# Kernel optimization log

Measured on AMD Instinct MI355X. Metric: run time of the kernel, lower is better.

## Reference

```python
import jax, jax.numpy as jnp
import numpy as np

L = 32      # num_layer
N_ORD = 64  # order_of_a_LTImodel
U = 64      # u_size
Y = 64      # y_size
T = 8192    # sequence length
SCALE = 0.05  # keep block-bidiagonal A spectrally stable over 8192 steps


def setup_inputs() -> dict:
    key = jax.random.key(0)
    k_u, k_a, k_b0, k_bl, k_c = jax.random.split(key, 5)
    inp = {
        "input": jax.random.normal(k_u, (T, U), dtype=jnp.float32),
        # per-layer A_i weights (diagonal blocks)
        "A_stack": jax.random.normal(k_a, (L, N_ORD, N_ORD), dtype=jnp.float32) * SCALE,
        # layer-0 B (maps u -> state)
        "B0": jax.random.normal(k_b0, (N_ORD, U), dtype=jnp.float32) * SCALE,
        # layer i>=1 B weights (sub-diagonal coupling blocks)
        "B_lower": jax.random.normal(k_bl, (L - 1, N_ORD, N_ORD), dtype=jnp.float32) * SCALE,
        # per-layer C_i weights, concatenated along columns in forward
        "C_stack": jax.random.normal(k_c, (L, Y, N_ORD), dtype=jnp.float32),
        # D is frozen zeros (feedthrough=False)
        "D_w": jnp.zeros((Y, U), dtype=jnp.float32),
    }
    return inp


def _assemble(A_stack, B0, B_lower, C_stack):
    l, n, _ = A_stack.shape
    S = l * n
    A = jnp.zeros((S, S), A_stack.dtype)
    for i in range(l):  # fixed small structural loop
        A = A.at[i * n:(i + 1) * n, i * n:(i + 1) * n].set(A_stack[i])
    for i in range(1, l):
        A = A.at[i * n:(i + 1) * n, (i - 1) * n:i * n].set(B_lower[i - 1])
    B = jnp.concatenate([B0, jnp.zeros((S - n, B0.shape[1]), B0.dtype)], axis=0)
    # torch.cat([C_i], dim=1): [Y, L*n]
    C = jnp.transpose(C_stack, (1, 0, 2)).reshape(C_stack.shape[1], S)
    return A, B, C


def reference(input, A_stack, B0, B_lower, C_stack, D_w):
    A, B, C = _assemble(A_stack, B0, B_lower, C_stack)
    S = A.shape[0]
    x0 = jnp.zeros((S,), input.dtype)

    def step(x, u):
        y = C @ x + D_w @ u      # output BEFORE state update (y_t uses x_t)
        x_next = A @ x + B @ u
        return x_next, y

    _, ys = jax.lax.scan(step, x0, input)
    return ys  # [T, Y]
```

## Files before the change

kernel.cpp:

```cpp
#include <hip/hip_runtime.h>


#define NO   64
#define TSEQ 8192
#define PAD8 40
#define PRX  8240
#define PBX  ((size_t)PRX*NO)
#define KQ   2048

typedef _Float16 h16;
typedef _Float16 h16x8 __attribute__((ext_vector_type(8)));
typedef float    f32x4 __attribute__((ext_vector_type(4)));

#define MFMA16(a,b,c) __builtin_amdgcn_mfma_f32_16x16x32_f16((a),(b),(c),0,0,0)
#define IMAX(a,b) ((a)>(b)?(a):(b))
#define IMIN(a,b) ((a)<(b)?(a):(b))

__global__ __launch_bounds__(256) void prep_build(
    const float* __restrict__ u, const float* __restrict__ B0,
    const float* __restrict__ Bl, const float* __restrict__ Cst,
    const float* __restrict__ Ast,
    h16* __restrict__ xq, h16* __restrict__ ccast,
    h16* __restrict__ SN, h16* __restrict__ ST,
    float* __restrict__ Dacc)
{
    __shared__ __align__(16) h16   Ah[64*72];
    __shared__ __align__(16) h16   kT[64*72];
    __shared__ __align__(16) float kf[64*68];
    const int tid = threadIdx.x;

    if (blockIdx.x < 32) {
        const int layer = blockIdx.x;
        const bool wantST = (layer & 3) == 0;
        const float* k0 = (layer == 0) ? B0 : (Bl + (size_t)(layer-1)*4096);
        const float* Aw = Ast + (size_t)layer*4096;
        for (int e8 = tid; e8 < 512; e8 += 256) {
            int n = e8 >> 3, m0 = (e8 & 7) << 3;
            f32x4 a0 = *(const f32x4*)&Aw[n*64 + m0];
            f32x4 a1 = *(const f32x4*)&Aw[n*64 + m0 + 4];
            h16 ah[8];
            #pragma unroll
            for (int t = 0; t < 4; t++) { ah[t] = (h16)a0[t]; ah[4+t] = (h16)a1[t]; }
            *(int4*)&Ah[n*72 + m0] = *(int4*)&ah[0];
            *(f32x4*)&kf[n*68 + m0]     = *(const f32x4*)&k0[n*64 + m0];
            *(f32x4*)&kf[n*68 + m0 + 4] = *(const f32x4*)&k0[n*64 + m0 + 4];
        }
        __syncthreads();
        const int wv = tid >> 6, lane = tid & 63, r = lane & 15, q = lane >> 4;
        const h16x8 a0 = *(const h16x8*)&Ah[(wv*16 + r)*72 + q*8];
        const h16x8 a1 = *(const h16x8*)&Ah[(wv*16 + r)*72 + 32 + q*8];
        for (int j = 0; j < 16; j++) {
            if (j > 0) {
                f32x4 acc[4] = {};
                #pragma unroll
                for (int c = 0; c < 4; c++) {
                    h16x8 b0 = *(const h16x8*)&kT[(c*16 + r)*72 + q*8];
                    h16x8 b1 = *(const h16x8*)&kT[(c*16 + r)*72 + 32 + q*8];
                    acc[c] = MFMA16(a0, b0, acc[c]);
                    acc[c] = MFMA16(a1, b1, acc[c]);
                }
                #pragma unroll
                for (int c = 0; c < 4; c++)
                    #pragma unroll
                    for (int g4 = 0; g4 < 4; g4++)
                        kf[(wv*16 + q*4 + g4)*68 + c*16 + r] = acc[c][g4];
                __syncthreads();
            }
            size_t base = (size_t)(layer*16 + j)*4096;
            for (int e8 = tid; e8 < 512; e8 += 256) {
                int n = e8 >> 3, m0 = (e8 & 7) << 3;
                f32x4 v0 = *(const f32x4*)&kf[n*68 + m0];
                f32x4 v1 = *(const f32x4*)&kf[n*68 + m0 + 4];
                h16 o[8];
                #pragma unroll
                for (int t = 0; t < 4; t++) { o[t] = (h16)v0[t]; o[4+t] = (h16)v1[t]; }
                if (!wantST)
                    *(int4*)&SN[base + (size_t)n*64 + m0] = *(int4*)&o[0];
                #pragma unroll
                for (int t = 0; t < 8; t++)
                    kT[(m0 + t)*72 + n] = o[t];
                if (wantST) {
                    h16 o2[8];
                    #pragma unroll
                    for (int t = 0; t < 8; t++) o2[t] = (h16)kf[(m0 + t)*68 + n];
                    *(int4*)&ST[base + (size_t)n*64 + m0] = *(int4*)&o2[0];
                }
            }
            __syncthreads();
        }
        return;
    }

    const int s1 = 320;
    const int s2 = 65536;
    const int s3 = 960;
    const int s4 = 16384;
    const int s6 = 262144;
    const int total = s1+s2+s3+s4+s6;
    const int4 z4 = make_int4(0,0,0,0);
    for (int e0 = (blockIdx.x - 32)*256 + tid; e0 < total; e0 += 512*256) {
        int e = e0;
        if (e < s1) { *(int4*)&xq[e*8] = z4; continue; }
        e -= s1;
        if (e < s2) {
            int el = e*8;
            f32x4 f0 = *(const f32x4*)&u[el];
            f32x4 f1 = *(const f32x4*)&u[el+4];
            h16 ov[8];
            #pragma unroll
            for (int j = 0; j < 4; j++) { ov[j] = (h16)f0[j]; ov[4+j] = (h16)f1[j]; }
            *(int4*)&xq[PAD8*NO + el] = *(int4*)&ov[0];
            continue;
        }
        e -= s2;
        if (e < s3) {
            int b = e / 320, off = (e % 320)*8;
            *(int4*)&xq[(size_t)(b+1)*PBX + off] = z4;
            continue;
        }
        e -= s3;
        if (e < s4) {
            int el = e*8;
            f32x4 f0 = *(const f32x4*)&Cst[el];
            f32x4 f1 = *(const f32x4*)&Cst[el+4];
            h16 ov[8];
            #pragma unroll
            for (int j = 0; j < 4; j++) { ov[j] = (h16)f0[j]; ov[4+j] = (h16)f1[j]; }
            *(int4*)&ccast[el] = *(int4*)&ov[0];
            continue;
        }
        e -= s4;
        *(int4*)&Dacc[e*4] = z4;
    }
}

__device__ __forceinline__ void comp_mm(const h16* __restrict__ X,
                                        const h16* __restrict__ Y,
                                        int wv, int r, int q, f32x4 acc[4])
{
    h16x8 a0 = *(const h16x8*)(X + (wv*16 + r)*64 + q*8);
    h16x8 a1 = *(const h16x8*)(X + (wv*16 + r)*64 + 32 + q*8);
    #pragma unroll
    for (int c = 0; c < 4; c++) {
        h16x8 b0 = *(const h16x8*)(Y + (c*16 + r)*64 + q*8);
        h16x8 b1 = *(const h16x8*)(Y + (c*16 + r)*64 + 32 + q*8);
        acc[c] = MFMA16(a0, b0, acc[c]);
        acc[c] = MFMA16(a1, b1, acc[c]);
    }
}
__device__ __forceinline__ void conv_loop(const h16* X, const h16* Y, int n,
                                          int wv, int r, int q, f32x4 acc[4])
{
    for (int it = 0; it < n; ++it) {
        comp_mm(X, Y, wv, r, q, acc);
        X += 4096; Y -= 4096;
    }
}
__device__ __forceinline__ void write_N(h16* o, int wv, int r, int q, const f32x4 acc[4])
{
    #pragma unroll
    for (int c = 0; c < 4; c++)
        #pragma unroll
        for (int g4 = 0; g4 < 4; g4++)
            o[(size_t)(wv*16 + q*4 + g4)*64 + c*16 + r] = (h16)acc[c][g4];
}
__device__ __forceinline__ void write_T(h16* o, int wv, int r, int q, const f32x4 acc[4])
{
    #pragma unroll
    for (int c = 0; c < 4; c++)
        #pragma unroll
        for (int g4 = 0; g4 < 4; g4++)
            o[(size_t)(c*16 + r)*64 + wv*16 + q*4 + g4] = (h16)acc[c][g4];
}

__global__ __launch_bounds__(256) void compose2(
    const h16* __restrict__ SN, const h16* __restrict__ ST,
    const h16* __restrict__ cc, h16* __restrict__ P2T,
    float* __restrict__ Dacc)
{
    const int tid = threadIdx.x, wv = tid>>6, lane = tid&63, r = lane&15, q = lane>>4;
    f32x4 acc[4] = {};
    int bid = blockIdx.x;
    if (bid < 248) {
        int g = bid / 31, m2 = bid % 31;
        int j0 = IMAX(0, m2 - 15);
        int j1 = IMIN(15, m2);
        conv_loop(SN + ((size_t)((4*g+1)*16) + j0)*4096,
                  ST + ((size_t)((4*g)*16) + (m2 - j0))*4096, j1-j0+1, wv, r, q, acc);
        write_T(P2T + ((size_t)(g*31 + m2))*4096, wv, r, q, acc);
    } else {
        int idx = bid - 248, g = idx >> 4, j = idx & 15;
        comp_mm(cc + (size_t)(4*g)*4096, ST + ((size_t)((4*g)*16) + j)*4096, wv, r, q, acc);
        float* Dd = Dacc + ((size_t)(g*32 + j))*4096;
        #pragma unroll
        for (int c = 0; c < 4; c++)
            #pragma unroll
            for (int g4 = 0; g4 < 4; g4++)
                atomicAdd(&Dd[(wv*16 + q*4 + g4)*64 + c*16 + r], acc[c][g4]);
    }
}

__global__ __launch_bounds__(256) void compose3(
    const h16* __restrict__ SN, const h16* __restrict__ cc,
    const h16* __restrict__ P2T, h16* __restrict__ P3T,
    float* __restrict__ Dacc)
{
    const int tid = threadIdx.x, wv = tid>>6, lane = tid&63, r = lane&15, q = lane>>4;
    f32x4 acc[4] = {};
    int bid = blockIdx.x;
    if (bid < 240) {
        int g = bid / 30, m3 = bid % 30;
        int j1 = IMIN(15, m3);
        conv_loop(SN + ((size_t)((4*g+2)*16))*4096,
                  P2T + ((size_t)(g*31 + m3))*4096, j1+1, wv, r, q, acc);
        write_T(P3T + ((size_t)(g*30 + m3))*4096, wv, r, q, acc);
    } else {
        int idx = bid - 240, g = idx / 31, m2 = idx % 31;
        comp_mm(cc + (size_t)(4*g+1)*4096, P2T + ((size_t)(g*31 + m2))*4096, wv, r, q, acc);
        float* Dd = Dacc + ((size_t)(g*32 + m2 + 1))*4096;
        #pragma unroll
        for (int c = 0; c < 4; c++)
            #pragma unroll
            for (int g4 = 0; g4 < 4; g4++)
                atomicAdd(&Dd[(wv*16 + q*4 + g4)*64 + c*16 + r], acc[c][g4]);
    }
}

__global__ __launch_bounds__(256) void compose4(
    const h16* __restrict__ SN, const h16* __restrict__ cc,
    const h16* __restrict__ P3T,
    h16* __restrict__ P4N, h16* __restrict__ P4T,
    float* __restrict__ Dacc)
{
    __shared__ h16 ldsT[64*72];
    const int tid = threadIdx.x, wv = tid>>6, lane = tid&63, r = lane&15, q = lane>>4;
    f32x4 acc[4] = {};
    int bid = blockIdx.x;
    if (bid < 232) {
        int g = bid / 29, m4 = bid % 29;
        int j1 = IMIN(15, m4);
        conv_loop(SN + ((size_t)((4*g+3)*16))*4096,
                  P3T + ((size_t)(g*30 + m4))*4096, j1+1, wv, r, q, acc);
        write_N(P4N + ((size_t)(g*29 + m4))*4096, wv, r, q, acc);
        write_T(P4T + ((size_t)(g*29 + m4))*4096, wv, r, q, acc);
        #pragma unroll
        for (int c = 0; c < 4; c++)
            #pragma unroll
            for (int g4 = 0; g4 < 4; g4++)
                ldsT[(c*16+r)*72 + wv*16 + q*4 + g4] = (h16)acc[c][g4];
        __syncthreads();
        f32x4 acc2[4] = {};
        const h16* Xc = cc + (size_t)(4*g+3)*4096;
        h16x8 a0 = *(const h16x8*)(Xc + (wv*16 + r)*64 + q*8);
        h16x8 a1 = *(const h16x8*)(Xc + (wv*16 + r)*64 + 32 + q*8);
        #pragma unroll
        for (int c = 0; c < 4; c++) {
            h16x8 b0 = *(const h16x8*)(&ldsT[(c*16+r)*72 + q*8]);
            h16x8 b1 = *(const h16x8*)(&ldsT[(c*16+r)*72 + 32 + q*8]);
            acc2[c] = MFMA16(a0, b0, acc2[c]);
            acc2[c] = MFMA16(a1, b1, acc2[c]);
        }
        float* Dd = Dacc + ((size_t)(g*32 + m4 + 3))*4096;
        #pragma unroll
        for (int c = 0; c < 4; c++)
            #pragma unroll
            for (int g4 = 0; g4 < 4; g4++)
                atomicAdd(&Dd[(wv*16 + q*4 + g4)*64 + c*16 + r], acc2[c][g4]);
    } else {
        int idx = bid - 232, g = idx / 30, m3 = idx % 30;
        comp_mm(cc + (size_t)(4*g+2)*4096, P3T + ((size_t)(g*30 + m3))*4096, wv, r, q, acc);
        float* Dd = Dacc + ((size_t)(g*32 + m3 + 2))*4096;
        #pragma unroll
        for (int c = 0; c < 4; c++)
            #pragma unroll
            for (int g4 = 0; g4 < 4; g4++)
                atomicAdd(&Dd[(wv*16 + q*4 + g4)*64 + c*16 + r], acc[c][g4]);
    }
}

__global__ __launch_bounds__(256) void castD(const float* __restrict__ Dacc,
                                             h16* __restrict__ D4N)
{
    const int total4 = 8*32*4096/4;
    for (int idx4 = blockIdx.x*256 + threadIdx.x; idx4 < total4; idx4 += 256*256) {
        int idx = idx4 << 2;
        f32x4 f = *(const f32x4*)&Dacc[idx];
        h16 o4[4];
        #pragma unroll
        for (int t = 0; t < 4; t++) o4[t] = (h16)f[t];
        *(int2*)&D4N[idx] = *(int2*)&o4[0];
    }
}

__global__ __launch_bounds__(256) void compose5(
    const h16* __restrict__ P4N, const h16* __restrict__ P4T,
    const h16* __restrict__ D4N, const float* __restrict__ D4F,
    h16* __restrict__ ktq8, h16* __restrict__ ktd8)
{
    const int tid = threadIdx.x, wv = tid>>6, lane = tid&63, r = lane&15, q = lane>>4;
    f32x4 acc[4] = {};
    int bid = blockIdx.x;
    if (bid < 128) {
        int o = bid >> 5, m = bid & 31, D = m + 8;
        int j0 = IMAX(4, D-32), j1 = IMIN(32, D-4);
        conv_loop(P4N + ((size_t)((2*o+1)*29) + (j0-4))*4096,
                  P4T + ((size_t)((2*o)*29) + (D-j0-4))*4096, j1-j0+1, wv, r, q, acc);
        h16* kq = ktq8 + (size_t)o*131072 + (size_t)(39 - D)*64;
        #pragma unroll
        for (int c = 0; c < 4; c++)
            #pragma unroll
            for (int g4 = 0; g4 < 4; g4++)
                kq[(size_t)(wv*16 + q*4 + g4)*KQ + c*16 + r] = (h16)acc[c][g4];
    } else {
        int idx = bid - 128, o = idx >> 5, m = idx & 31, D = m + 1;
        int n = D - 4;
        if (n > 0)
            conv_loop(D4N + ((size_t)((2*o+1)*32))*4096,
                      P4T + ((size_t)((2*o)*29) + (D-1-4))*4096, n, wv, r, q, acc);
        const float* DF = D4F + ((size_t)((2*o)*32 + D-1))*4096;
        #pragma unroll
        for (int c = 0; c < 4; c++)
            #pragma unroll
            for (int g4 = 0; g4 < 4; g4++)
                acc[c][g4] += DF[(size_t)(wv*16 + q*4 + g4)*64 + c*16 + r];
        h16* kd = ktd8 + (size_t)o*131072 + (size_t)(32 - D)*64;
        #pragma unroll
        for (int c = 0; c < 4; c++)
            #pragma unroll
            for (int g4 = 0; g4 < 4; g4++)
                kd[(size_t)(wv*16 + q*4 + g4)*KQ + c*16 + r] = (h16)acc[c][g4];
    }
}

template<int WRST>
__global__ __launch_bounds__(512) void stage8(
    const h16* __restrict__ pin, h16* __restrict__ pout,
    const h16* __restrict__ ktqg, const h16* __restrict__ ktdg,
    float* __restrict__ out, int first)
{
    __shared__ __align__(16) h16   win[104*72];
    __shared__ __align__(16) float red[4*32*68];
    const int tid = threadIdx.x;
    const size_t t0 = (size_t)blockIdx.x * 64;

    for (int e = tid; e < 104*8; e += 512) {
        int rr = e >> 3, cc = e & 7;
        *(int4*)&win[rr*72 + cc*8] = *(const int4*)&pin[(t0 + 1 + rr)*64 + cc*8];
    }
    __syncthreads();

    const int wv = tid >> 6, lane = tid & 63, r = lane & 15, q = lane >> 4;
    const int half = wv >> 2, kq = wv & 3;
    const bool active = WRST || (half == 1);
    f32x4 acc[2][2][4] = {};
    if (active) {
        const h16* kb = half ? ktdg : ktqg;
        const h16* abase = &win[(r + kq*8 + (half ? 7 : 0))*72 + q*8];
        const h16* bbase = kb + (size_t)r*KQ + kq*512 + q*8;
#define LDA(st, s, ls) (*(const h16x8*)(abase + ((st)*32 + (s)*16 + ((ls)>>1))*72 + ((ls)&1)*32))
#define LDB(c, ls) (*(const h16x8*)(bbase + (size_t)(c)*(16*KQ) + (ls)*32))
        h16x8 a[2][2][2], b[2][4];
        #pragma unroll
        for (int sl = 0; sl < 2; sl++) {
            #pragma unroll
            for (int st = 0; st < 2; st++)
                #pragma unroll
                for (int s = 0; s < 2; s++) a[sl][st][s] = LDA(st, s, sl);
            #pragma unroll
            for (int c = 0; c < 4; c++) b[sl][c] = LDB(c, sl);
        }
        #pragma unroll
        for (int ls = 0; ls < 16; ls++) {
            h16x8 ca[2][2], cb[4];
            #pragma unroll
            for (int st = 0; st < 2; st++)
                #pragma unroll
                for (int s = 0; s < 2; s++) ca[st][s] = a[ls&1][st][s];
            #pragma unroll
            for (int c = 0; c < 4; c++) cb[c] = b[ls&1][c];
            if (ls < 14) {
                #pragma unroll
                for (int st = 0; st < 2; st++)
                    #pragma unroll
                    for (int s = 0; s < 2; s++) a[ls&1][st][s] = LDA(st, s, ls+2);
                #pragma unroll
                for (int c = 0; c < 4; c++) b[ls&1][c] = LDB(c, ls+2);
            }
            #pragma unroll
            for (int st = 0; st < 2; st++)
                #pragma unroll
                for (int s = 0; s < 2; s++)
                    #pragma unroll
                    for (int c = 0; c < 4; c++)
                        acc[st][s][c] = MFMA16(ca[st][s], cb[c], acc[st][s][c]);
        }
#undef LDA
#undef LDB
    }

    const int rh = half * (2*32*68);
    #pragma unroll
    for (int st = 0; st < 2; st++) {
        __syncthreads();
        if (active && kq >= 2) {
            float* myred = red + rh + (kq-2)*(32*68);
            #pragma unroll
            for (int s2 = 0; s2 < 2; s2++)
                #pragma unroll
                for (int c = 0; c < 4; c++)
                    #pragma unroll
                    for (int g4 = 0; g4 < 4; g4++)
                        myred[(s2*16 + q*4 + g4)*68 + c*16 + r] = acc[st][s2][c][g4];
        }
        __syncthreads();
        if (active && kq < 2) {
            float* myred = red + rh + kq*(32*68);
            #pragma unroll
            for (int s2 = 0; s2 < 2; s2++)
                #pragma unroll
                for (int c = 0; c < 4; c++)
                    #pragma unroll
                    for (int g4 = 0; g4 < 4; g4++)
                        myred[(s2*16 + q*4 + g4)*68 + c*16 + r] += acc[st][s2][c][g4];
        }
        __syncthreads();
        if (WRST && tid < 256) {
            int orow = tid >> 3, cb2 = (tid & 7) << 3;
            f32x4 u0 = *(const f32x4*)&red[orow*68 + cb2];
            f32x4 u1 = *(const f32x4*)&red[orow*68 + cb2 + 4];
            f32x4 v0 = *(const f32x4*)&red[32*68 + orow*68 + cb2];
            f32x4 v1 = *(const f32x4*)&red[32*68 + orow*68 + cb2 + 4];
            u0 += v0; u1 += v1;
            h16 ov[8];
            #pragma unroll
            for (int j = 0; j < 4; j++) { ov[j] = (h16)u0[j]; ov[4+j] = (h16)u1[j]; }
            *(int4*)&pout[(PAD8 + t0 + st*32 + orow)*64 + cb2] = *(int4*)&ov[0];
        }
        if (tid >= 256) {
            int t2 = tid - 256;
            int orow = t2 >> 3, cb2 = (t2 & 7) << 3;
            const float* base = red + 2*32*68;
            f32x4 u0 = *(const f32x4*)&base[orow*68 + cb2];
            f32x4 u1 = *(const f32x4*)&base[orow*68 + cb2 + 4];
            f32x4 v0 = *(const f32x4*)&base[32*68 + orow*68 + cb2];
            f32x4 v1 = *(const f32x4*)&base[32*68 + orow*68 + cb2 + 4];
            u0 += v0; u1 += v1;
            float* op = out + (t0 + st*32 + orow)*64 + cb2;
            if (first) {
                *(f32x4*)op = u0; *(f32x4*)(op+4) = u1;
            } else {
                f32x4 o0 = *(f32x4*)op, o1 = *(f32x4*)(op+4);
                o0 += u0; o1 += u1;
                *(f32x4*)op = o0; *(f32x4*)(op+4) = o1;
            }
        }
    }
}

extern "C" void kernel_launch(void* const* d_in, const int* in_sizes, int n_in,
                              void* d_out, int out_size, void* d_ws, size_t ws_size,
                              hipStream_t stream)
{
    const float* u   = (const float*)d_in[0];
    const float* Ast = (const float*)d_in[1];
    const float* B0  = (const float*)d_in[2];
    const float* Bl  = (const float*)d_in[3];
    const float* Cst = (const float*)d_in[4];
    float* out = (float*)d_out;
    (void)in_sizes; (void)n_in; (void)out_size; (void)ws_size;

    char* ws = (char*)d_ws;
    h16*   xq   = (h16*)  (ws + 0);
    h16*   ccast= (h16*)  (ws + 4218880);
    h16*   SN   = (h16*)  (ws + 4481024);
    h16*   ST   = (h16*)  (ws + 8675328);
    h16*   P2T  = (h16*)  (ws + 12869632);
    h16*   P3T  = (h16*)  (ws + 14901248);
    h16*   P4N  = (h16*)  (ws + 16867328);
    h16*   P4T  = (h16*)  (ws + 18767872);
    float* Dacc = (float*)(ws + 20668416);
    h16*   D4N  = (h16*)  (ws + 24862720);
    h16*   ktq8 = (h16*)  (ws + 26959872);
    h16*   ktd8 = (h16*)  (ws + 28008448);

    prep_build<<<544, 256, 0, stream>>>(u, B0, Bl, Cst, Ast, xq, ccast, SN, ST, Dacc);
    compose2<<<376, 256, 0, stream>>>(SN, ST, ccast, P2T, Dacc);
    compose3<<<488, 256, 0, stream>>>(SN, ccast, P2T, P3T, Dacc);
    compose4<<<472, 256, 0, stream>>>(SN, ccast, P3T, P4N, P4T, Dacc);
    castD<<<256, 256, 0, stream>>>(Dacc, D4N);
    compose5<<<256, 256, 0, stream>>>(P4N, P4T, D4N, Dacc, ktq8, ktd8);
    for (int g = 0; g < 3; g++) {
        stage8<1><<<TSEQ/64, 512, 0, stream>>>(xq + (size_t)g*PBX, xq + (size_t)(g+1)*PBX,
                                               ktq8 + (size_t)g*131072, ktd8 + (size_t)g*131072,
                                               out, g == 0);
    }
    stage8<0><<<TSEQ/64, 512, 0, stream>>>(xq + (size_t)3*PBX, xq,
                                           ktq8 + (size_t)3*131072, ktd8 + (size_t)3*131072,
                                           out, 0);
}
```

Measured before the change: 262.8 us.

## Compose 16-layer kernels and replace four stage8 passes with two-stage pipeline

Adds another composition level (compose6) that merges the 8-layer block kernels into 16-layer transfer kernels. The sequence pass then needs one wider stage (stage1) and one output-only stage (stage2) instead of four sequential stage8 launches. The aim is to cut the intermediate state round trips and the launch count of the sequence sweep. In exchange it adds precomposition work and longer convolution windows (K widths 2560 and 3072), and the extra fp16 rounding in the deeper composition may affect accuracy.

```diff
diff --git a/kernel.cpp b/kernel.cpp
--- a/kernel.cpp
+++ b/kernel.cpp
@@ -3,10 +3,11 @@
 
 #define NO   64
 #define TSEQ 8192
-#define PAD8 40
-#define PRX  8240
-#define PBX  ((size_t)PRX*NO)
-#define KQ   2048
+#define PAD16 56
+#define PR16 8288
+#define PBX  ((size_t)PR16*NO)
+#define KQ16 2560
+#define KY16 3072
 
 typedef _Float16 h16;
 typedef _Float16 h16x8 __attribute__((ext_vector_type(8)));
@@ -20,7 +21,8 @@
     const float* __restrict__ u, const float* __restrict__ B0,
     const float* __restrict__ Bl, const float* __restrict__ Cst,
     const float* __restrict__ Ast,
-    h16* __restrict__ xq, h16* __restrict__ ccast,
+    h16* __restrict__ uq, h16* __restrict__ x16,
+    h16* __restrict__ ccast,
     h16* __restrict__ SN, h16* __restrict__ ST,
     float* __restrict__ Dacc)
 {
@@ -91,16 +93,16 @@
         return;
     }
 
-    const int s1 = 320;
+    const int s1 = 448;
     const int s2 = 65536;
-    const int s3 = 960;
+    const int s3 = 448;
     const int s4 = 16384;
     const int s6 = 262144;
     const int total = s1+s2+s3+s4+s6;
     const int4 z4 = make_int4(0,0,0,0);
     for (int e0 = (blockIdx.x - 32)*256 + tid; e0 < total; e0 += 512*256) {
         int e = e0;
-        if (e < s1) { *(int4*)&xq[e*8] = z4; continue; }
+        if (e < s1) { *(int4*)&uq[e*8] = z4; continue; }
         e -= s1;
         if (e < s2) {
             int el = e*8;
@@ -109,15 +111,11 @@
             h16 ov[8];
             #pragma unroll
             for (int j = 0; j < 4; j++) { ov[j] = (h16)f0[j]; ov[4+j] = (h16)f1[j]; }
-            *(int4*)&xq[PAD8*NO + el] = *(int4*)&ov[0];
+            *(int4*)&uq[PAD16*NO + el] = *(int4*)&ov[0];
             continue;
         }
         e -= s2;
-        if (e < s3) {
-            int b = e / 320, off = (e % 320)*8;
-            *(int4*)&xq[(size_t)(b+1)*PBX + off] = z4;
-            continue;
-        }
+        if (e < s3) { *(int4*)&x16[e*8] = z4; continue; }
         e -= s3;
         if (e < s4) {
             int el = e*8;
@@ -171,6 +169,14 @@
         #pragma unroll
         for (int g4 = 0; g4 < 4; g4++)
             o[(size_t)(c*16 + r)*64 + wv*16 + q*4 + g4] = (h16)acc[c][g4];
+}
+__device__ __forceinline__ void write_F(float* o, int wv, int r, int q, const f32x4 acc[4])
+{
+    #pragma unroll
+    for (int c = 0; c < 4; c++)
+        #pragma unroll
+        for (int g4 = 0; g4 < 4; g4++)
+            o[(size_t)(wv*16 + q*4 + g4)*64 + c*16 + r] = acc[c][g4];
 }
 
 __global__ __launch_bounds__(256) void compose2(
@@ -295,7 +301,8 @@
 __global__ __launch_bounds__(256) void compose5(
     const h16* __restrict__ P4N, const h16* __restrict__ P4T,
     const h16* __restrict__ D4N, const float* __restrict__ D4F,
-    h16* __restrict__ ktq8, h16* __restrict__ ktd8)
+    h16* __restrict__ P8N, h16* __restrict__ P8T,
+    h16* __restrict__ D8N, float* __restrict__ D8F)
 {
     const int tid = threadIdx.x, wv = tid>>6, lane = tid&63, r = lane&15, q = lane>>4;
     f32x4 acc[4] = {};
@@ -305,12 +312,8 @@
         int j0 = IMAX(4, D-32), j1 = IMIN(32, D-4);
         conv_loop(P4N + ((size_t)((2*o+1)*29) + (j0-4))*4096,
                   P4T + ((size_t)((2*o)*29) + (D-j0-4))*4096, j1-j0+1, wv, r, q, acc);
-        h16* kq = ktq8 + (size_t)o*131072 + (size_t)(39 - D)*64;
-        #pragma unroll
-        for (int c = 0; c < 4; c++)
-            #pragma unroll
-            for (int g4 = 0; g4 < 4; g4++)
-                kq[(size_t)(wv*16 + q*4 + g4)*KQ + c*16 + r] = (h16)acc[c][g4];
+        write_N(P8N + ((size_t)(o*32 + m))*4096, wv, r, q, acc);
+        write_T(P8T + ((size_t)(o*32 + m))*4096, wv, r, q, acc);
     } else {
         int idx = bid - 128, o = idx >> 5, m = idx & 31, D = m + 1;
         int n = D - 4;
@@ -323,42 +326,77 @@
             #pragma unroll
             for (int g4 = 0; g4 < 4; g4++)
                 acc[c][g4] += DF[(size_t)(wv*16 + q*4 + g4)*64 + c*16 + r];
-        h16* kd = ktd8 + (size_t)o*131072 + (size_t)(32 - D)*64;
-        #pragma unroll
-        for (int c = 0; c < 4; c++)
-            #pragma unroll
-            for (int g4 = 0; g4 < 4; g4++)
-                kd[(size_t)(wv*16 + q*4 + g4)*KQ + c*16 + r] = (h16)acc[c][g4];
-    }
-}
-
-template<int WRST>
-__global__ __launch_bounds__(512) void stage8(
-    const h16* __restrict__ pin, h16* __restrict__ pout,
-    const h16* __restrict__ ktqg, const h16* __restrict__ ktdg,
-    float* __restrict__ out, int first)
-{
-    __shared__ __align__(16) h16   win[104*72];
+        write_N(D8N + ((size_t)(o*32 + m))*4096, wv, r, q, acc);
+        write_F(D8F + ((size_t)(o*32 + m))*4096, wv, r, q, acc);
+    }
+}
+
+__global__ __launch_bounds__(256) void compose6(
+    const h16* __restrict__ P8N, const h16* __restrict__ P8T,
+    const h16* __restrict__ D8N, const float* __restrict__ D8F,
+    h16* __restrict__ ktq16, h16* __restrict__ ktd16)
+{
+    const int tid = threadIdx.x, wv = tid>>6, lane = tid&63, r = lane&15, q = lane>>4;
+    f32x4 acc[4] = {};
+    int bid = blockIdx.x;
+    if (bid < 40) {
+        int D = bid + 16;
+        int j0 = IMAX(8, D-39), j1 = IMIN(39, D-8);
+        conv_loop(P8N + ((size_t)(1*32) + (j0-8))*4096,
+                  P8T + ((size_t)(0*32) + (D-j0-8))*4096, j1-j0+1, wv, r, q, acc);
+        h16* kq = ktq16 + (size_t)(55 - D)*64;
+        #pragma unroll
+        for (int c = 0; c < 4; c++)
+            #pragma unroll
+            for (int g4 = 0; g4 < 4; g4++)
+                kq[(size_t)(wv*16 + q*4 + g4)*KQ16 + c*16 + r] = (h16)acc[c][g4];
+    } else {
+        int idx = bid - 40, g = idx / 48, m = idx % 48, D = m + 1;
+        int j0 = IMAX(1, D-39), j1 = IMIN(32, D-8);
+        if (j1 >= j0)
+            conv_loop(D8N + ((size_t)((2*g+1)*32) + (j0-1))*4096,
+                      P8T + ((size_t)((2*g)*32) + (D-j0-8))*4096, j1-j0+1, wv, r, q, acc);
+        if (D <= 32) {
+            const float* DF = D8F + ((size_t)((2*g)*32 + D-1))*4096;
+            #pragma unroll
+            for (int c = 0; c < 4; c++)
+                #pragma unroll
+                for (int g4 = 0; g4 < 4; g4++)
+                    acc[c][g4] += DF[(size_t)(wv*16 + q*4 + g4)*64 + c*16 + r];
+        }
+        h16* kd = ktd16 + (size_t)g*(64*KY16) + (size_t)(48 - D)*64;
+        #pragma unroll
+        for (int c = 0; c < 4; c++)
+            #pragma unroll
+            for (int g4 = 0; g4 < 4; g4++)
+                kd[(size_t)(wv*16 + q*4 + g4)*KY16 + c*16 + r] = (h16)acc[c][g4];
+    }
+}
+
+__global__ __launch_bounds__(512) void stage1(
+    const h16* __restrict__ uq, h16* __restrict__ x16,
+    const h16* __restrict__ ktq, const h16* __restrict__ ktd,
+    float* __restrict__ out)
+{
+    __shared__ __align__(16) h16   win[120*72];
     __shared__ __align__(16) float red[4*32*68];
     const int tid = threadIdx.x;
     const size_t t0 = (size_t)blockIdx.x * 64;
 
-    for (int e = tid; e < 104*8; e += 512) {
+    for (int e = tid; e < 120*8; e += 512) {
         int rr = e >> 3, cc = e & 7;
-        *(int4*)&win[rr*72 + cc*8] = *(const int4*)&pin[(t0 + 1 + rr)*64 + cc*8];
+        *(int4*)&win[rr*72 + cc*8] = *(const int4*)&uq[(t0 + 1 + rr)*64 + cc*8];
     }
     __syncthreads();
 
     const int wv = tid >> 6, lane = tid & 63, r = lane & 15, q = lane >> 4;
     const int half = wv >> 2, kq = wv & 3;
-    const bool active = WRST || (half == 1);
     f32x4 acc[2][2][4] = {};
-    if (active) {
-        const h16* kb = half ? ktdg : ktqg;
-        const h16* abase = &win[(r + kq*8 + (half ? 7 : 0))*72 + q*8];
-        const h16* bbase = kb + (size_t)r*KQ + kq*512 + q*8;
+    if (half == 0) {
+        const h16* abase = &win[(r + kq*10)*72 + q*8];
+        const h16* bbase = ktq + (size_t)r*KQ16 + kq*640 + q*8;
 #define LDA(st, s, ls) (*(const h16x8*)(abase + ((st)*32 + (s)*16 + ((ls)>>1))*72 + ((ls)&1)*32))
-#define LDB(c, ls) (*(const h16x8*)(bbase + (size_t)(c)*(16*KQ) + (ls)*32))
+#define LDB(c, ls) (*(const h16x8*)(bbase + (size_t)(c)*(16*KQ16) + (ls)*32))
         h16x8 a[2][2][2], b[2][4];
         #pragma unroll
         for (int sl = 0; sl < 2; sl++) {
@@ -370,7 +408,7 @@
             for (int c = 0; c < 4; c++) b[sl][c] = LDB(c, sl);
         }
         #pragma unroll
-        for (int ls = 0; ls < 16; ls++) {
+        for (int ls = 0; ls < 20; ls++) {
             h16x8 ca[2][2], cb[4];
             #pragma unroll
             for (int st = 0; st < 2; st++)
@@ -378,7 +416,49 @@
                 for (int s = 0; s < 2; s++) ca[st][s] = a[ls&1][st][s];
             #pragma unroll
             for (int c = 0; c < 4; c++) cb[c] = b[ls&1][c];
-            if (ls < 14) {
+            if (ls < 18) {
+                #pragma unroll
+                for (int st = 0; st < 2; st++)
+                    #pragma unroll
+                    for (int s = 0; s < 2; s++) a[ls&1][st][s] = LDA(st, s, ls+2);
+                #pragma unroll
+                for (int c = 0; c < 4; c++) b[ls&1][c] = LDB(c, ls+2);
+            }
+            #pragma unroll
+            for (int st = 0; st < 2; st++)
+                #pragma unroll
+                for (int s = 0; s < 2; s++)
+                    #pragma unroll
+                    for (int c = 0; c < 4; c++)
+                        acc[st][s][c] = MFMA16(ca[st][s], cb[c], acc[st][s][c]);
+        }
+#undef LDA
+#undef LDB
+    } else {
+        const h16* abase = &win[(r + kq*12 + 7)*72 + q*8];
+        const h16* bbase = ktd + (size_t)r*KY16 + kq*768 + q*8;
+#define LDA(st, s, ls) (*(const h16x8*)(abase + ((st)*32 + (s)*16 + ((ls)>>1))*72 + ((ls)&1)*32))
+#define LDB(c, ls) (*(const h16x8*)(bbase + (size_t)(c)*(16*KY16) + (ls)*32))
+        h16x8 a[2][2][2], b[2][4];
+        #pragma unroll
+        for (int sl = 0; sl < 2; sl++) {
+            #pragma unroll
+            for (int st = 0; st < 2; st++)
+                #pragma unroll
+                for (int s = 0; s < 2; s++) a[sl][st][s] = LDA(st, s, sl);
+            #pragma unroll
+            for (int c = 0; c < 4; c++) b[sl][c] = LDB(c, sl);
+        }
+        #pragma unroll
+        for (int ls = 0; ls < 24; ls++) {
+            h16x8 ca[2][2], cb[4];
+            #pragma unroll
+            for (int st = 0; st < 2; st++)
+                #pragma unroll
+                for (int s = 0; s < 2; s++) ca[st][s] = a[ls&1][st][s];
+            #pragma unroll
+            for (int c = 0; c < 4; c++) cb[c] = b[ls&1][c];
+            if (ls < 22) {
                 #pragma unroll
                 for (int st = 0; st < 2; st++)
                     #pragma unroll
@@ -402,7 +482,7 @@
     #pragma unroll
     for (int st = 0; st < 2; st++) {
         __syncthreads();
-        if (active && kq >= 2) {
+        if (kq >= 2) {
             float* myred = red + rh + (kq-2)*(32*68);
             #pragma unroll
             for (int s2 = 0; s2 < 2; s2++)
@@ -413,7 +493,7 @@
                         myred[(s2*16 + q*4 + g4)*68 + c*16 + r] = acc[st][s2][c][g4];
         }
         __syncthreads();
-        if (active && kq < 2) {
+        if (kq < 2) {
             float* myred = red + rh + kq*(32*68);
             #pragma unroll
             for (int s2 = 0; s2 < 2; s2++)
@@ -424,7 +504,7 @@
                         myred[(s2*16 + q*4 + g4)*68 + c*16 + r] += acc[st][s2][c][g4];
         }
         __syncthreads();
-        if (WRST && tid < 256) {
+        if (tid < 256) {
             int orow = tid >> 3, cb2 = (tid & 7) << 3;
             f32x4 u0 = *(const f32x4*)&red[orow*68 + cb2];
             f32x4 u1 = *(const f32x4*)&red[orow*68 + cb2 + 4];
@@ -434,9 +514,8 @@
             h16 ov[8];
             #pragma unroll
             for (int j = 0; j < 4; j++) { ov[j] = (h16)u0[j]; ov[4+j] = (h16)u1[j]; }
-            *(int4*)&pout[(PAD8 + t0 + st*32 + orow)*64 + cb2] = *(int4*)&ov[0];
-        }
-        if (tid >= 256) {
+            *(int4*)&x16[(PAD16 + t0 + st*32 + orow)*64 + cb2] = *(int4*)&ov[0];
+        } else {
             int t2 = tid - 256;
             int orow = t2 >> 3, cb2 = (t2 & 7) << 3;
             const float* base = red + 2*32*68;
@@ -446,14 +525,99 @@
             f32x4 v1 = *(const f32x4*)&base[32*68 + orow*68 + cb2 + 4];
             u0 += v0; u1 += v1;
             float* op = out + (t0 + st*32 + orow)*64 + cb2;
-            if (first) {
-                *(f32x4*)op = u0; *(f32x4*)(op+4) = u1;
-            } else {
-                f32x4 o0 = *(f32x4*)op, o1 = *(f32x4*)(op+4);
-                o0 += u0; o1 += u1;
-                *(f32x4*)op = o0; *(f32x4*)(op+4) = o1;
-            }
-        }
+            *(f32x4*)op = u0; *(f32x4*)(op+4) = u1;
+        }
+    }
+}
+
+__global__ __launch_bounds__(512) void stage2(
+    const h16* __restrict__ x16, const h16* __restrict__ ktd,
+    float* __restrict__ out)
+{
+    __shared__ __align__(16) h16   win[80*72];
+    __shared__ __align__(16) float red[4*32*68];
+    const int tid = threadIdx.x;
+    const size_t t0 = (size_t)blockIdx.x * 32;
+
+    for (int e = tid; e < 80*8; e += 512) {
+        int rr = e >> 3, cc = e & 7;
+        *(int4*)&win[rr*72 + cc*8] = *(const int4*)&x16[(t0 + 8 + rr)*64 + cc*8];
+    }
+    __syncthreads();
+
+    const int wv = tid >> 6, lane = tid & 63, r = lane & 15, q = lane >> 4;
+    const h16* abase = &win[(r + wv*6)*72 + q*8];
+    const h16* bbase = ktd + (size_t)r*KY16 + wv*384 + q*8;
+#define LDA(s, ls) (*(const h16x8*)(abase + ((s)*16 + ((ls)>>1))*72 + ((ls)&1)*32))
+#define LDB(c, ls) (*(const h16x8*)(bbase + (size_t)(c)*(16*KY16) + (ls)*32))
+    f32x4 acc[2][4] = {};
+    h16x8 a[2][2], b[2][4];
+    #pragma unroll
+    for (int sl = 0; sl < 2; sl++) {
+        #pragma unroll
+        for (int s = 0; s < 2; s++) a[sl][s] = LDA(s, sl);
+        #pragma unroll
+        for (int c = 0; c < 4; c++) b[sl][c] = LDB(c, sl);
+    }
+    #pragma unroll
+    for (int ls = 0; ls < 12; ls++) {
+        h16x8 ca[2], cb[4];
+        #pragma unroll
+        for (int s = 0; s < 2; s++) ca[s] = a[ls&1][s];
+        #pragma unroll
+        for (int c = 0; c < 4; c++) cb[c] = b[ls&1][c];
+        if (ls < 10) {
+            #pragma unroll
+            for (int s = 0; s < 2; s++) a[ls&1][s] = LDA(s, ls+2);
+            #pragma unroll
+            for (int c = 0; c < 4; c++) b[ls&1][c] = LDB(c, ls+2);
+        }
+        #pragma unroll
+        for (int s = 0; s < 2; s++)
+            #pragma unroll
+            for (int c = 0; c < 4; c++)
+                acc[s][c] = MFMA16(ca[s], cb[c], acc[s][c]);
+    }
+#undef LDA
+#undef LDB
+    const int kq = wv & 3;
+    const int rh = (wv >> 2) * (2*32*68);
+    __syncthreads();
+    if (kq >= 2) {
+        float* myred = red + rh + (kq-2)*(32*68);
+        #pragma unroll
+        for (int s2 = 0; s2 < 2; s2++)
+            #pragma unroll
+            for (int c = 0; c < 4; c++)
+                #pragma unroll
+                for (int g4 = 0; g4 < 4; g4++)
+                    myred[(s2*16 + q*4 + g4)*68 + c*16 + r] = acc[s2][c][g4];
+    }
+    __syncthreads();
+    if (kq < 2) {
+        float* myred = red + rh + kq*(32*68);
+        #pragma unroll
+        for (int s2 = 0; s2 < 2; s2++)
+            #pragma unroll
+            for (int c = 0; c < 4; c++)
+                #pragma unroll
+                for (int g4 = 0; g4 < 4; g4++)
+                    myred[(s2*16 + q*4 + g4)*68 + c*16 + r] += acc[s2][c][g4];
+    }
+    __syncthreads();
+    if (tid < 256) {
+        int orow = tid >> 3, cb2 = (tid & 7) << 3;
+        f32x4 u0 = *(const f32x4*)&red[orow*68 + cb2];
+        f32x4 u1 = *(const f32x4*)&red[orow*68 + cb2 + 4];
+        #pragma unroll
+        for (int bnk = 1; bnk < 4; bnk++) {
+            u0 += *(const f32x4*)&red[bnk*(32*68) + orow*68 + cb2];
+            u1 += *(const f32x4*)&red[bnk*(32*68) + orow*68 + cb2 + 4];
+        }
+        float* op = out + (t0 + orow)*64 + cb2;
+        f32x4 o0 = *(f32x4*)op, o1 = *(f32x4*)(op+4);
+        o0 += u0; o1 += u1;
+        *(f32x4*)op = o0; *(f32x4*)(op+4) = o1;
     }
 }
 
@@ -470,31 +634,31 @@
     (void)in_sizes; (void)n_in; (void)out_size; (void)ws_size;
 
     char* ws = (char*)d_ws;
-    h16*   xq   = (h16*)  (ws + 0);
-    h16*   ccast= (h16*)  (ws + 4218880);
-    h16*   SN   = (h16*)  (ws + 4481024);
-    h16*   ST   = (h16*)  (ws + 8675328);
-    h16*   P2T  = (h16*)  (ws + 12869632);
-    h16*   P3T  = (h16*)  (ws + 14901248);
-    h16*   P4N  = (h16*)  (ws + 16867328);
-    h16*   P4T  = (h16*)  (ws + 18767872);
-    float* Dacc = (float*)(ws + 20668416);
-    h16*   D4N  = (h16*)  (ws + 24862720);
-    h16*   ktq8 = (h16*)  (ws + 26959872);
-    h16*   ktd8 = (h16*)  (ws + 28008448);
-
-    prep_build<<<544, 256, 0, stream>>>(u, B0, Bl, Cst, Ast, xq, ccast, SN, ST, Dacc);
+    h16*   uq   = (h16*)  (ws + 0);
+    h16*   x16  = (h16*)  (ws + 1060864);
+    h16*   ccast= (h16*)  (ws + 2121728);
+    h16*   SN   = (h16*)  (ws + 2383872);
+    h16*   ST   = (h16*)  (ws + 6578176);
+    h16*   P2T  = (h16*)  (ws + 10772480);
+    h16*   P3T  = (h16*)  (ws + 12804096);
+    h16*   P4N  = (h16*)  (ws + 14770176);
+    h16*   P4T  = (h16*)  (ws + 16670720);
+    float* Dacc = (float*)(ws + 18571264);
+    h16*   D4N  = (h16*)  (ws + 22765568);
+    h16*   P8N  = (h16*)  (ws + 24862720);
+    h16*   P8T  = (h16*)  (ws + 25911296);
+    h16*   D8N  = (h16*)  (ws + 26959872);
+    float* D8F  = (float*)(ws + 28008448);
+    h16*   ktq16= (h16*)  (ws + 30105600);
+    h16*   ktd16= (h16*)  (ws + 30433280);
+
+    prep_build<<<544, 256, 0, stream>>>(u, B0, Bl, Cst, Ast, uq, x16, ccast, SN, ST, Dacc);
     compose2<<<376, 256, 0, stream>>>(SN, ST, ccast, P2T, Dacc);
     compose3<<<488, 256, 0, stream>>>(SN, ccast, P2T, P3T, Dacc);
     compose4<<<472, 256, 0, stream>>>(SN, ccast, P3T, P4N, P4T, Dacc);
     castD<<<256, 256, 0, stream>>>(Dacc, D4N);
-    compose5<<<256, 256, 0, stream>>>(P4N, P4T, D4N, Dacc, ktq8, ktd8);
-    for (int g = 0; g < 3; g++) {
-        stage8<1><<<TSEQ/64, 512, 0, stream>>>(xq + (size_t)g*PBX, xq + (size_t)(g+1)*PBX,
-                                               ktq8 + (size_t)g*131072, ktd8 + (size_t)g*131072,
-                                               out, g == 0);
-    }
-    stage8<0><<<TSEQ/64, 512, 0, stream>>>(xq + (size_t)3*PBX, xq,
-                                           ktq8 + (size_t)3*131072, ktd8 + (size_t)3*131072,
-                                           out, 0);
-}
+    compose5<<<256, 256, 0, stream>>>(P4N, P4T, D4N, Dacc, P8N, P8T, D8N, D8F);
+    compose6<<<136, 256, 0, stream>>>(P8N, P8T, D8N, D8F, ktq16, ktd16);
+    stage1<<<TSEQ/64, 512, 0, stream>>>(uq, x16, ktq16, ktd16, out);
+    stage2<<<TSEQ/32, 512, 0, stream>>>(x16, ktd16 + (size_t)64*KY16, out);
+}
```

New measurement: 268.4 us. 1.02x slower.
